# Kernel optimization log

Hardware: AMD Instinct MI355X
Metric: run time of the kernel (lower is better)

## Reference

```python
import jax
import jax.numpy as jnp
import numpy as np
from jax import lax

B, L, A, C = 32, 128, 64, 128  # batch, length, n_agents, channels (in == out)
KT = 3                          # temporal kernel size, padding (KT-1)//2 keeps length


def setup_inputs() -> dict:
    key = jax.random.key(0)
    k1, k2, k3 = jax.random.split(key, 3)
    x = jax.random.normal(k1, (B, L, A, C), dtype=jnp.float32)
    # Conv2d weight [out_ch, in_ch, kt, 1] and bias, kaiming-ish scale
    W = jax.random.normal(k2, (C, C, KT, 1), dtype=jnp.float32) * (1.0 / np.sqrt(C * KT))
    b = jax.random.normal(k3, (C,), dtype=jnp.float32) * 0.01
    return {"x": x, "W": W, "b": b}


def reference(x, W, b):
    # x: [B, L, A, C] -> [B, C, L, A] (torch NCHW layout with H=time, W=agents)
    length, n_agents = x.shape[1], x.shape[2]
    xc = jnp.transpose(x, (0, 3, 1, 2))
    res = xc  # residual is identity (input_dim == output_dim, t_stride == 1)
    pad_t = (KT - 1) // 2
    y = lax.conv_general_dilated(
        xc, W,
        window_strides=(1, 1),
        padding=[(pad_t, pad_t), (0, 0)],
        dimension_numbers=("NCHW", "OIHW", "NCHW"),
    ) + b[None, :, None, None]  # [B, C, L, A]
    # Dense graph g[t,a,t',a'] = 1 iff t==t' or a==a'.  einsum('ncv,vw->ncw', x, g)
    # is exactly: sum over same time (all agents) + sum over same agent (all times) - self.
    agent_sum = jnp.sum(y, axis=3, keepdims=True)  # [B, C, L, 1]
    time_sum = jnp.sum(y, axis=2, keepdims=True)   # [B, C, 1, A]
    scale = (length + n_agents - 2) ** 0.5
    g = (agent_sum + time_sum - y) / scale
    out = jax.nn.relu(g + res)
    return jnp.transpose(out, (0, 2, 3, 1))  # [B, L, A, C]
```

## Files before the change

### kernel.cpp

```cpp
#include <hip/hip_runtime.h>
#include <stdint.h>


typedef __attribute__((ext_vector_type(8))) short bf16x8;
typedef __attribute__((ext_vector_type(4))) float f32x4;

__device__ __forceinline__ uint32_t f2bf(float f) {
    union { float f; uint32_t u; } v; v.f = f;
    return (v.u + 0x7FFFu + ((v.u >> 16) & 1u)) >> 16;
}
__device__ __forceinline__ float bf2f(uint32_t h) {
    union { uint32_t u; float f; } v; v.u = h << 16; return v.f;
}
__device__ __forceinline__ uint32_t pk2(float lo, float hi) {
    return f2bf(lo) | (f2bf(hi) << 16);
}
__device__ __forceinline__ void gll16(const void* g, void* l) {
    __builtin_amdgcn_global_load_lds((const __attribute__((address_space(1))) void*)g,
                                     (__attribute__((address_space(3))) void*)l, 16, 0, 0);
}

__global__ __launch_bounds__(256) void prep_kernel(
    const float* __restrict__ x, uint16_t* __restrict__ x16, uint16_t* __restrict__ xa16,
    const float* __restrict__ W, uint16_t* __restrict__ wp, float* __restrict__ xt)
{
    const int tid = threadIdx.x;
    const int bid = blockIdx.x;
    if (bid >= 4352) {
        const int idx = bid - 4352;
        const int a = idx & 63, b = idx >> 6;
        const int ci8 = (tid & 15) * 8, tg = tid >> 4;
        const float* base = x + ((size_t)(b * 128 + tg) * 64 + a) * 128 + ci8;
        float s[8];
        #pragma unroll
        for (int j = 0; j < 8; ++j) s[j] = 0.f;
        #pragma unroll
        for (int r = 0; r < 8; ++r) {
            const float* p = base + (size_t)r * 16 * 8192;
            const float4 v0 = *(const float4*)p;
            const float4 v1 = *(const float4*)(p + 4);
            s[0] += v0.x; s[1] += v0.y; s[2] += v0.z; s[3] += v0.w;
            s[4] += v1.x; s[5] += v1.y; s[6] += v1.z; s[7] += v1.w;
        }
        __shared__ float redx[16][128];
        *(float4*)&redx[tg][ci8]     = make_float4(s[0], s[1], s[2], s[3]);
        *(float4*)&redx[tg][ci8 + 4] = make_float4(s[4], s[5], s[6], s[7]);
        __syncthreads();
        if (tid < 128) {
            float v = 0.f;
            #pragma unroll
            for (int i = 0; i < 16; ++i) v += redx[i][tid];
            xt[(size_t)idx * 128 + tid] = v;
        }
        return;
    }
    if (bid >= 4160) {
        int o = (bid - 4160) * 256 + tid;
        int i = o & 7, lane = (o >> 3) & 63, nt = (o >> 9) & 7, ks = (o >> 12) & 3, d = o >> 14;
        int ci = ks * 32 + (lane >> 4) * 8 + i;
        int co = nt * 16 + (lane & 15);
        wp[o] = (uint16_t)f2bf(W[(co * 128 + ci) * 3 + d]);
        return;
    }
    const int b = bid / 130, tp = bid - b * 130;
    uint16_t* xo = x16 + (size_t)bid * 8192;
    if (tp == 0 || tp == 129) {
        const uint4 z = make_uint4(0, 0, 0, 0);
        #pragma unroll
        for (int k = 0; k < 4; ++k) *(uint4*)(xo + tid * 32 + k * 8) = z;
        if (tid < 16) *(uint4*)(xa16 + (size_t)bid * 128 + tid * 8) = z;
        return;
    }
    const int t = tp - 1;
    const int ci8 = (tid & 15) * 8, ag = tid >> 4;
    const float* xr = x + (size_t)(b * 128 + t) * 8192;
    float s[8];
    #pragma unroll
    for (int j = 0; j < 8; ++j) s[j] = 0.f;
    #pragma unroll
    for (int r = 0; r < 4; ++r) {
        const int a = ag * 4 + r;
        const float4 v0 = *(const float4*)(xr + a * 128 + ci8);
        const float4 v1 = *(const float4*)(xr + a * 128 + ci8 + 4);
        s[0] += v0.x; s[1] += v0.y; s[2] += v0.z; s[3] += v0.w;
        s[4] += v1.x; s[5] += v1.y; s[6] += v1.z; s[7] += v1.w;
        uint4 p;
        p.x = pk2(v0.x, v0.y); p.y = pk2(v0.z, v0.w);
        p.z = pk2(v1.x, v1.y); p.w = pk2(v1.z, v1.w);
        *(uint4*)(xo + a * 128 + ci8) = p;
    }
    __shared__ float red[16][128];
    *(float4*)&red[ag][ci8]     = make_float4(s[0], s[1], s[2], s[3]);
    *(float4*)&red[ag][ci8 + 4] = make_float4(s[4], s[5], s[6], s[7]);
    __syncthreads();
    if (tid < 128) {
        float v = 0.f;
        #pragma unroll
        for (int i = 0; i < 16; ++i) v += red[i][tid];
        xa16[(size_t)bid * 128 + tid] = (uint16_t)f2bf(v);
    }
}

__global__ __launch_bounds__(256, 2) void sums_kernel(
    const uint16_t* __restrict__ xa16, const float* __restrict__ xt,
    const uint16_t* __restrict__ x16, const uint16_t* __restrict__ wp,
    const float* __restrict__ bias, float* __restrict__ asum, float* __restrict__ tsum)
{
    __shared__ __align__(16) uint16_t slab[130 * 128];
    const int tid = threadIdx.x;
    const int lane = tid & 63, wid = tid >> 6;
    const int wm = wid >> 1, wn = wid & 1;
    const int lr = lane & 15, lg = lane >> 4;
    f32x4 acc[4][4];
    #pragma unroll
    for (int mi = 0; mi < 4; ++mi)
        #pragma unroll
        for (int ni = 0; ni < 4; ++ni) acc[mi][ni] = (f32x4)0.f;

    if (blockIdx.x < 32) {
        const int b = blockIdx.x;
        #pragma unroll
        for (int it = 0; it < 9; ++it) {
            const int gg = it * 256 + tid;
            if (gg < 2080) {
                const int row = gg >> 4, sp = gg & 15;
                const int sl = sp ^ (row & 7);
                *(uint4*)(slab + gg * 8) =
                    *(const uint4*)(xa16 + (size_t)(b * 130 + row) * 128 + sl * 8);
            }
        }
        __syncthreads();
        #pragma unroll
        for (int g = 0; g < 4; ++g)
            #pragma unroll
            for (int d = 0; d < 3; ++d) {
                bf16x8 bq[4], af[4];
                #pragma unroll
                for (int ni = 0; ni < 4; ++ni)
                    bq[ni] = *(const bf16x8*)(wp + (size_t)((((d * 4 + g) * 8) + wn * 4 + ni) * 64 + lane) * 8);
                #pragma unroll
                for (int mi = 0; mi < 4; ++mi) {
                    const int row = wm * 64 + mi * 16 + lr + d;
                    af[mi] = *(const bf16x8*)(slab + row * 128 + ((g * 4 + lg) ^ (row & 7)) * 8);
                }
                #pragma unroll
                for (int mi = 0; mi < 4; ++mi)
                    #pragma unroll
                    for (int ni = 0; ni < 4; ++ni)
                        acc[mi][ni] = __builtin_amdgcn_mfma_f32_16x16x32_bf16(af[mi], bq[ni], acc[mi][ni], 0, 0, 0);
            }
        #pragma unroll
        for (int ni = 0; ni < 4; ++ni) {
            const int col = wn * 64 + ni * 16 + lr;
            const float bv = 64.f * bias[col];
            #pragma unroll
            for (int mi = 0; mi < 4; ++mi)
                #pragma unroll
                for (int j = 0; j < 4; ++j) {
                    const int t = wm * 64 + mi * 16 + lg * 4 + j;
                    asum[((size_t)b * 128 + t) * 128 + col] = acc[mi][ni][j] + bv;
                }
        }
        return;
    }

    const int bid = blockIdx.x - 32;
    const int r = tid >> 1, h = tid & 1;
    const int grow = bid * 128 + r, sb = grow >> 6, sa = grow & 63;
    #pragma unroll
    for (int d = 0; d < 3; ++d) {
        {
            const float* Sp = xt + (size_t)grow * 128 + h * 64;
            const uint16_t* Ep = x16 + ((size_t)(sb * 130 + (d == 0 ? 128 : 1)) * 64 + sa) * 128 + h * 64;
            #pragma unroll
            for (int k = 0; k < 8; ++k) {
                float4 f0 = *(const float4*)(Sp + k * 8);
                float4 f1 = *(const float4*)(Sp + k * 8 + 4);
                if (d != 1) {
                    const uint4 e = *(const uint4*)(Ep + k * 8);
                    f0.x -= bf2f(e.x & 0xFFFFu); f0.y -= bf2f(e.x >> 16);
                    f0.z -= bf2f(e.y & 0xFFFFu); f0.w -= bf2f(e.y >> 16);
                    f1.x -= bf2f(e.z & 0xFFFFu); f1.y -= bf2f(e.z >> 16);
                    f1.z -= bf2f(e.w & 0xFFFFu); f1.w -= bf2f(e.w >> 16);
                }
                uint4 o;
                o.x = pk2(f0.x, f0.y); o.y = pk2(f0.z, f0.w);
                o.z = pk2(f1.x, f1.y); o.w = pk2(f1.z, f1.w);
                const int sl = h * 8 + k;
                *(uint4*)(slab + r * 128 + (sl ^ (r & 7)) * 8) = o;
            }
        }
        __syncthreads();
        #pragma unroll
        for (int g = 0; g < 4; ++g) {
            bf16x8 bq[4], af[4];
            #pragma unroll
            for (int ni = 0; ni < 4; ++ni)
                bq[ni] = *(const bf16x8*)(wp + (size_t)((((d * 4 + g) * 8) + wn * 4 + ni) * 64 + lane) * 8);
            #pragma unroll
            for (int mi = 0; mi < 4; ++mi) {
                const int row = wm * 64 + mi * 16 + lr;
                af[mi] = *(const bf16x8*)(slab + row * 128 + ((g * 4 + lg) ^ (row & 7)) * 8);
            }
            #pragma unroll
            for (int mi = 0; mi < 4; ++mi)
                #pragma unroll
                for (int ni = 0; ni < 4; ++ni)
                    acc[mi][ni] = __builtin_amdgcn_mfma_f32_16x16x32_bf16(af[mi], bq[ni], acc[mi][ni], 0, 0, 0);
        }
        __syncthreads();
    }
    #pragma unroll
    for (int ni = 0; ni < 4; ++ni) {
        const int col = wn * 64 + ni * 16 + lr;
        const float bv = 128.f * bias[col];
        #pragma unroll
        for (int mi = 0; mi < 4; ++mi)
            #pragma unroll
            for (int j = 0; j < 4; ++j) {
                const int rg = bid * 128 + wm * 64 + mi * 16 + lg * 4 + j;
                tsum[(size_t)rg * 128 + col] = acc[mi][ni][j] + bv;
            }
    }
}

__global__ __launch_bounds__(512, 6) void conv_kernel(
    const uint16_t* __restrict__ x16, const uint16_t* __restrict__ wp,
    const float* __restrict__ bias, const float* __restrict__ asum,
    const float* __restrict__ tsum, float* __restrict__ out)
{
    __shared__ __align__(16) uint16_t slab[2][192 * 64];
    const int tid = threadIdx.x;
    const int raw = blockIdx.x;
    const int bid = (raw & 7) * 512 + (raw >> 3);
    const int b = bid >> 7, t = bid & 127;
    const int lane = tid & 63, wid = tid >> 6;
    const int lr = lane & 15, lg = lane >> 4;

    f32x4 acc[4];
    #pragma unroll
    for (int mi = 0; mi < 4; ++mi) acc[mi] = (f32x4)0.f;

#define STAGE(c) do {                                                          \
    _Pragma("unroll")                                                          \
    for (int k = 0; k < 3; ++k) {                                              \
        const int row = wid * 24 + k * 8 + (lane >> 3);                        \
        const int gran = (lane & 7) ^ (row & 7);                               \
        const uint16_t* src = x16 +                                            \
            ((size_t)((b * 130 + t + (row >> 6)) * 64 + (row & 63))) * 128 +   \
            (c) * 64 + gran * 8;                                               \
        gll16(src, &slab[c][wid * 1536 + k * 512]);                            \
    } } while (0)

#define MFMA_CHUNK(c) do {                                                     \
    _Pragma("unroll")                                                          \
    for (int d = 0; d < 3; ++d)                                                \
        _Pragma("unroll")                                                      \
        for (int g2 = 0; g2 < 2; ++g2) {                                       \
            const int ks = (c) * 2 + g2;                                       \
            bf16x8 bq, af[4];                                                  \
            bq = *(const bf16x8*)(wp +                                         \
                (size_t)((((d * 4 + ks) * 8) + wid) * 64 + lane) * 8);         \
            _Pragma("unroll")                                                  \
            for (int mi = 0; mi < 4; ++mi) {                                   \
                const int row = d * 64 + mi * 16 + lr;                         \
                af[mi] = *(const bf16x8*)(&slab[c][row * 64 +                  \
                    (((g2 * 4 + lg) ^ (row & 7)) * 8)]);                       \
            }                                                                  \
            _Pragma("unroll")                                                  \
            for (int mi = 0; mi < 4; ++mi)                                     \
                acc[mi] = __builtin_amdgcn_mfma_f32_16x16x32_bf16(             \
                    af[mi], bq, acc[mi], 0, 0, 0);                             \
        } } while (0)

    STAGE(0);
    __syncthreads();
    STAGE(1);
    MFMA_CHUNK(0);
    __syncthreads();
    MFMA_CHUNK(1);
    __syncthreads();

#undef STAGE
#undef MFMA_CHUNK

    {
        const int col = wid * 16 + lr;
        const float bv = bias[col];
        const int cbuf = col >> 6, cl = col & 63;
        #pragma unroll
        for (int mi = 0; mi < 4; ++mi)
            #pragma unroll
            for (int j = 0; j < 4; ++j) {
                const int a = mi * 16 + lg * 4 + j;
                slab[cbuf][a * 64 + (cl ^ ((a & 7) << 3))] = (uint16_t)f2bf(acc[mi][j] + bv);
            }
    }
    __syncthreads();

    {
        const float inv = 0.07254762501100116f;
        const int cg = tid & 15, rb = tid >> 4;
        const int cbuf = cg >> 3, cl8 = (cg & 7) * 8;
        const float* ap = asum + ((size_t)(b * 128 + t)) * 128 + cg * 8;
        const float4 as0 = *(const float4*)ap, as1 = *(const float4*)(ap + 4);
        const float av[8] = {as0.x, as0.y, as0.z, as0.w, as1.x, as1.y, as1.z, as1.w};
        #pragma unroll
        for (int j = 0; j < 2; ++j) {
            const int a = j * 32 + rb;
            const int swz = cl8 ^ ((a & 7) << 3);
            const uint4 yv = *(const uint4*)(&slab[cbuf][a * 64 + swz]);
            const uint4 xv = *(const uint4*)(&slab[cbuf][(64 + a) * 64 + swz]);
            const float* tp = tsum + ((size_t)(b * 64 + a)) * 128 + cg * 8;
            const float4 ts0 = *(const float4*)tp, ts1 = *(const float4*)(tp + 4);
            float yy[8], xx[8];
            yy[0] = bf2f(yv.x & 0xFFFFu); yy[1] = bf2f(yv.x >> 16);
            yy[2] = bf2f(yv.y & 0xFFFFu); yy[3] = bf2f(yv.y >> 16);
            yy[4] = bf2f(yv.z & 0xFFFFu); yy[5] = bf2f(yv.z >> 16);
            yy[6] = bf2f(yv.w & 0xFFFFu); yy[7] = bf2f(yv.w >> 16);
            xx[0] = bf2f(xv.x & 0xFFFFu); xx[1] = bf2f(xv.x >> 16);
            xx[2] = bf2f(xv.y & 0xFFFFu); xx[3] = bf2f(xv.y >> 16);
            xx[4] = bf2f(xv.z & 0xFFFFu); xx[5] = bf2f(xv.z >> 16);
            xx[6] = bf2f(xv.w & 0xFFFFu); xx[7] = bf2f(xv.w >> 16);
            const float tv[8] = {ts0.x, ts0.y, ts0.z, ts0.w, ts1.x, ts1.y, ts1.z, ts1.w};
            float o[8];
            #pragma unroll
            for (int i = 0; i < 8; ++i) {
                const float gg = (av[i] + tv[i] - yy[i]) * inv + xx[i];
                o[i] = gg > 0.f ? gg : 0.f;
            }
            float* op = out + ((size_t)((b * 128 + t) * 64 + a)) * 128 + cg * 8;
            *(float4*)op       = make_float4(o[0], o[1], o[2], o[3]);
            *(float4*)(op + 4) = make_float4(o[4], o[5], o[6], o[7]);
        }
    }
}

extern "C" void kernel_launch(void* const* d_in, const int* in_sizes, int n_in,
                              void* d_out, int out_size, void* d_ws, size_t ws_size,
                              hipStream_t stream) {
    const float* x    = (const float*)d_in[0];
    const float* W    = (const float*)d_in[1];
    const float* bias = (const float*)d_in[2];
    float* out = (float*)d_out;

    char* ws = (char*)d_ws;
    uint16_t* x16  = (uint16_t*)(ws);
    uint16_t* wp   = (uint16_t*)(ws + 68157440);
    uint16_t* xa16 = (uint16_t*)(ws + 68157440 + 98304);
    float* xt      = (float*)(ws + 68157440 + 98304 + 1064960);
    float* asum    = (float*)(ws + 68157440 + 98304 + 1064960 + 1048576);
    float* tsum    = (float*)(ws + 68157440 + 98304 + 1064960 + 1048576 + 2097152);

    prep_kernel <<<6400, 256, 0, stream>>>(x, x16, xa16, W, wp, xt);
    sums_kernel <<<48,   256, 0, stream>>>(xa16, xt, x16, wp, bias, asum, tsum);
    conv_kernel <<<4096, 512, 0, stream>>>(x16, wp, bias, asum, tsum, out);
}
```

Measured before the change: 129.7 us.

## Drop bf16 copy of input; convert fp32 to bf16 inside conv staging

Removes the intermediate bf16 padded copy of x, so the conv kernel loads fp32 x directly and converts it to bf16 while staging into LDS, with zeros for the time-padding rows. The time and agent reductions are fused into a single pass over x that writes per-group partial time sums, followed by a small second-stage reduction kernel. This is meant to eliminate the large write and re-read of x16 and a duplicate read of x. In exchange, conv reads twice as many bytes per tile and gives up the async global-to-LDS loads in favour of register loads plus LDS stores.

```diff
diff --git a/kernel.cpp b/kernel.cpp
--- a/kernel.cpp
+++ b/kernel.cpp
@@ -15,95 +15,96 @@
 __device__ __forceinline__ uint32_t pk2(float lo, float hi) {
     return f2bf(lo) | (f2bf(hi) << 16);
 }
-__device__ __forceinline__ void gll16(const void* g, void* l) {
-    __builtin_amdgcn_global_load_lds((const __attribute__((address_space(1))) void*)g,
-                                     (__attribute__((address_space(3))) void*)l, 16, 0, 0);
-}
-
-__global__ __launch_bounds__(256) void prep_kernel(
-    const float* __restrict__ x, uint16_t* __restrict__ x16, uint16_t* __restrict__ xa16,
-    const float* __restrict__ W, uint16_t* __restrict__ wp, float* __restrict__ xt)
+
+__global__ __launch_bounds__(256) void red_kernel(
+    const float* __restrict__ x, uint16_t* __restrict__ xa16, float* __restrict__ xt_part,
+    const float* __restrict__ W, uint16_t* __restrict__ wp)
 {
     const int tid = threadIdx.x;
     const int bid = blockIdx.x;
-    if (bid >= 4352) {
-        const int idx = bid - 4352;
-        const int a = idx & 63, b = idx >> 6;
-        const int ci8 = (tid & 15) * 8, tg = tid >> 4;
-        const float* base = x + ((size_t)(b * 128 + tg) * 64 + a) * 128 + ci8;
-        float s[8];
-        #pragma unroll
-        for (int j = 0; j < 8; ++j) s[j] = 0.f;
-        #pragma unroll
-        for (int r = 0; r < 8; ++r) {
-            const float* p = base + (size_t)r * 16 * 8192;
-            const float4 v0 = *(const float4*)p;
-            const float4 v1 = *(const float4*)(p + 4);
-            s[0] += v0.x; s[1] += v0.y; s[2] += v0.z; s[3] += v0.w;
-            s[4] += v1.x; s[5] += v1.y; s[6] += v1.z; s[7] += v1.w;
-        }
-        __shared__ float redx[16][128];
-        *(float4*)&redx[tg][ci8]     = make_float4(s[0], s[1], s[2], s[3]);
-        *(float4*)&redx[tg][ci8 + 4] = make_float4(s[4], s[5], s[6], s[7]);
-        __syncthreads();
-        if (tid < 128) {
-            float v = 0.f;
-            #pragma unroll
-            for (int i = 0; i < 16; ++i) v += redx[i][tid];
-            xt[(size_t)idx * 128 + tid] = v;
-        }
-        return;
-    }
-    if (bid >= 4160) {
-        int o = (bid - 4160) * 256 + tid;
+    if (bid >= 512) {
+        int o = (bid - 512) * 256 + tid;
         int i = o & 7, lane = (o >> 3) & 63, nt = (o >> 9) & 7, ks = (o >> 12) & 3, d = o >> 14;
         int ci = ks * 32 + (lane >> 4) * 8 + i;
         int co = nt * 16 + (lane & 15);
         wp[o] = (uint16_t)f2bf(W[(co * 128 + ci) * 3 + d]);
         return;
     }
-    const int b = bid / 130, tp = bid - b * 130;
-    uint16_t* xo = x16 + (size_t)bid * 8192;
-    if (tp == 0 || tp == 129) {
-        const uint4 z = make_uint4(0, 0, 0, 0);
-        #pragma unroll
-        for (int k = 0; k < 4; ++k) *(uint4*)(xo + tid * 32 + k * 8) = z;
-        if (tid < 16) *(uint4*)(xa16 + (size_t)bid * 128 + tid * 8) = z;
-        return;
-    }
-    const int t = tp - 1;
+    const int b = bid >> 4, g = bid & 15;
     const int ci8 = (tid & 15) * 8, ag = tid >> 4;
-    const float* xr = x + (size_t)(b * 128 + t) * 8192;
+    __shared__ float red[16][128];
+
+    float xtl[4][8];
+    #pragma unroll
+    for (int r = 0; r < 4; ++r)
+        #pragma unroll
+        for (int j = 0; j < 8; ++j) xtl[r][j] = 0.f;
+
+    #pragma unroll
+    for (int ti = 0; ti < 8; ++ti) {
+        const int t = g * 8 + ti;
+        const float* xr = x + ((size_t)(b * 128 + t) * 64) * 128;
+        float s[8];
+        #pragma unroll
+        for (int j = 0; j < 8; ++j) s[j] = 0.f;
+        #pragma unroll
+        for (int r = 0; r < 4; ++r) {
+            const int a = ag * 4 + r;
+            const float4 v0 = *(const float4*)(xr + a * 128 + ci8);
+            const float4 v1 = *(const float4*)(xr + a * 128 + ci8 + 4);
+            s[0] += v0.x; s[1] += v0.y; s[2] += v0.z; s[3] += v0.w;
+            s[4] += v1.x; s[5] += v1.y; s[6] += v1.z; s[7] += v1.w;
+            xtl[r][0] += v0.x; xtl[r][1] += v0.y; xtl[r][2] += v0.z; xtl[r][3] += v0.w;
+            xtl[r][4] += v1.x; xtl[r][5] += v1.y; xtl[r][6] += v1.z; xtl[r][7] += v1.w;
+        }
+        *(float4*)&red[ag][ci8]     = make_float4(s[0], s[1], s[2], s[3]);
+        *(float4*)&red[ag][ci8 + 4] = make_float4(s[4], s[5], s[6], s[7]);
+        __syncthreads();
+        if (tid < 128) {
+            float v = 0.f;
+            #pragma unroll
+            for (int i = 0; i < 16; ++i) v += red[i][tid];
+            xa16[(size_t)(b * 130 + t + 1) * 128 + tid] = (uint16_t)f2bf(v);
+        }
+        __syncthreads();
+    }
+    if (g == 0 && tid < 16)
+        *(uint4*)(xa16 + (size_t)(b * 130) * 128 + tid * 8) = make_uint4(0, 0, 0, 0);
+    if (g == 15 && tid < 16)
+        *(uint4*)(xa16 + (size_t)(b * 130 + 129) * 128 + tid * 8) = make_uint4(0, 0, 0, 0);
+    #pragma unroll
+    for (int r = 0; r < 4; ++r) {
+        float* p = xt_part + (((size_t)(b * 16 + g) * 64 + ag * 4 + r) * 128) + ci8;
+        *(float4*)p       = make_float4(xtl[r][0], xtl[r][1], xtl[r][2], xtl[r][3]);
+        *(float4*)(p + 4) = make_float4(xtl[r][4], xtl[r][5], xtl[r][6], xtl[r][7]);
+    }
+}
+
+__global__ __launch_bounds__(256) void xtr_kernel(
+    const float* __restrict__ xt_part, float* __restrict__ xt)
+{
+    const int idx = blockIdx.x * 256 + threadIdx.x;
+    const int row = idx >> 4, ci8 = (idx & 15) * 8;
+    const int b = row >> 6, a = row & 63;
     float s[8];
     #pragma unroll
     for (int j = 0; j < 8; ++j) s[j] = 0.f;
     #pragma unroll
-    for (int r = 0; r < 4; ++r) {
-        const int a = ag * 4 + r;
-        const float4 v0 = *(const float4*)(xr + a * 128 + ci8);
-        const float4 v1 = *(const float4*)(xr + a * 128 + ci8 + 4);
+    for (int g2 = 0; g2 < 16; ++g2) {
+        const float* p = xt_part + (((size_t)(b * 16 + g2) * 64 + a) * 128) + ci8;
+        const float4 v0 = *(const float4*)p;
+        const float4 v1 = *(const float4*)(p + 4);
         s[0] += v0.x; s[1] += v0.y; s[2] += v0.z; s[3] += v0.w;
         s[4] += v1.x; s[5] += v1.y; s[6] += v1.z; s[7] += v1.w;
-        uint4 p;
-        p.x = pk2(v0.x, v0.y); p.y = pk2(v0.z, v0.w);
-        p.z = pk2(v1.x, v1.y); p.w = pk2(v1.z, v1.w);
-        *(uint4*)(xo + a * 128 + ci8) = p;
-    }
-    __shared__ float red[16][128];
-    *(float4*)&red[ag][ci8]     = make_float4(s[0], s[1], s[2], s[3]);
-    *(float4*)&red[ag][ci8 + 4] = make_float4(s[4], s[5], s[6], s[7]);
-    __syncthreads();
-    if (tid < 128) {
-        float v = 0.f;
-        #pragma unroll
-        for (int i = 0; i < 16; ++i) v += red[i][tid];
-        xa16[(size_t)bid * 128 + tid] = (uint16_t)f2bf(v);
-    }
+    }
+    float* q = xt + (size_t)row * 128 + ci8;
+    *(float4*)q       = make_float4(s[0], s[1], s[2], s[3]);
+    *(float4*)(q + 4) = make_float4(s[4], s[5], s[6], s[7]);
 }
 
 __global__ __launch_bounds__(256, 2) void sums_kernel(
     const uint16_t* __restrict__ xa16, const float* __restrict__ xt,
-    const uint16_t* __restrict__ x16, const uint16_t* __restrict__ wp,
+    const float* __restrict__ x, const uint16_t* __restrict__ wp,
     const float* __restrict__ bias, float* __restrict__ asum, float* __restrict__ tsum)
 {
     __shared__ __align__(16) uint16_t slab[130 * 128];
@@ -171,17 +172,16 @@
     for (int d = 0; d < 3; ++d) {
         {
             const float* Sp = xt + (size_t)grow * 128 + h * 64;
-            const uint16_t* Ep = x16 + ((size_t)(sb * 130 + (d == 0 ? 128 : 1)) * 64 + sa) * 128 + h * 64;
+            const float* Ep = x + ((size_t)((sb * 128 + (d == 0 ? 127 : 0)) * 64 + sa)) * 128 + h * 64;
             #pragma unroll
             for (int k = 0; k < 8; ++k) {
                 float4 f0 = *(const float4*)(Sp + k * 8);
                 float4 f1 = *(const float4*)(Sp + k * 8 + 4);
                 if (d != 1) {
-                    const uint4 e = *(const uint4*)(Ep + k * 8);
-                    f0.x -= bf2f(e.x & 0xFFFFu); f0.y -= bf2f(e.x >> 16);
-                    f0.z -= bf2f(e.y & 0xFFFFu); f0.w -= bf2f(e.y >> 16);
-                    f1.x -= bf2f(e.z & 0xFFFFu); f1.y -= bf2f(e.z >> 16);
-                    f1.z -= bf2f(e.w & 0xFFFFu); f1.w -= bf2f(e.w >> 16);
+                    const float4 e0 = *(const float4*)(Ep + k * 8);
+                    const float4 e1 = *(const float4*)(Ep + k * 8 + 4);
+                    f0.x -= e0.x; f0.y -= e0.y; f0.z -= e0.z; f0.w -= e0.w;
+                    f1.x -= e1.x; f1.y -= e1.y; f1.z -= e1.z; f1.w -= e1.w;
                 }
                 uint4 o;
                 o.x = pk2(f0.x, f0.y); o.y = pk2(f0.z, f0.w);
@@ -225,7 +225,7 @@
 }
 
 __global__ __launch_bounds__(512, 6) void conv_kernel(
-    const uint16_t* __restrict__ x16, const uint16_t* __restrict__ wp,
+    const float* __restrict__ x, const uint16_t* __restrict__ wp,
     const float* __restrict__ bias, const float* __restrict__ asum,
     const float* __restrict__ tsum, float* __restrict__ out)
 {
@@ -244,12 +244,21 @@
 #define STAGE(c) do {                                                          \
     _Pragma("unroll")                                                          \
     for (int k = 0; k < 3; ++k) {                                              \
-        const int row = wid * 24 + k * 8 + (lane >> 3);                        \
-        const int gran = (lane & 7) ^ (row & 7);                               \
-        const uint16_t* src = x16 +                                            \
-            ((size_t)((b * 130 + t + (row >> 6)) * 64 + (row & 63))) * 128 +   \
-            (c) * 64 + gran * 8;                                               \
-        gll16(src, &slab[c][wid * 1536 + k * 512]);                            \
+        const int ro  = lane >> 3;                                             \
+        const int row = wid * 24 + k * 8 + ro;                                 \
+        const int gl  = (lane & 7) ^ ro;                                       \
+        const int tloc = t + (row >> 6) - 1;                                   \
+        uint4 o4 = make_uint4(0, 0, 0, 0);                                     \
+        if ((unsigned)tloc < 128u) {                                           \
+            const float* s_ = x +                                              \
+                ((size_t)((b * 128 + tloc) * 64 + (row & 63))) * 128 +         \
+                (c) * 64 + gl * 8;                                             \
+            const float4 v0 = *(const float4*)s_;                              \
+            const float4 v1 = *(const float4*)(s_ + 4);                        \
+            o4.x = pk2(v0.x, v0.y); o4.y = pk2(v0.z, v0.w);                    \
+            o4.z = pk2(v1.x, v1.y); o4.w = pk2(v1.z, v1.w);                    \
+        }                                                                      \
+        *(uint4*)(&slab[c][wid * 1536 + k * 512 + lane * 8]) = o4;             \
     } } while (0)
 
 #define MFMA_CHUNK(c) do {                                                     \
@@ -345,14 +354,15 @@
     float* out = (float*)d_out;
 
     char* ws = (char*)d_ws;
-    uint16_t* x16  = (uint16_t*)(ws);
-    uint16_t* wp   = (uint16_t*)(ws + 68157440);
-    uint16_t* xa16 = (uint16_t*)(ws + 68157440 + 98304);
-    float* xt      = (float*)(ws + 68157440 + 98304 + 1064960);
-    float* asum    = (float*)(ws + 68157440 + 98304 + 1064960 + 1048576);
-    float* tsum    = (float*)(ws + 68157440 + 98304 + 1064960 + 1048576 + 2097152);
-
-    prep_kernel <<<6400, 256, 0, stream>>>(x, x16, xa16, W, wp, xt);
-    sums_kernel <<<48,   256, 0, stream>>>(xa16, xt, x16, wp, bias, asum, tsum);
-    conv_kernel <<<4096, 512, 0, stream>>>(x16, wp, bias, asum, tsum, out);
-}
+    uint16_t* wp    = (uint16_t*)(ws);
+    uint16_t* xa16  = (uint16_t*)(ws + 98304);
+    float* xt_part  = (float*)(ws + 98304 + 1064960);
+    float* xt       = (float*)(ws + 98304 + 1064960 + 16777216);
+    float* asum     = (float*)(ws + 98304 + 1064960 + 16777216 + 1048576);
+    float* tsum     = (float*)(ws + 98304 + 1064960 + 16777216 + 1048576 + 2097152);
+
+    red_kernel  <<<704,  256, 0, stream>>>(x, xa16, xt_part, W, wp);
+    xtr_kernel  <<<128,  256, 0, stream>>>(xt_part, xt);
+    sums_kernel <<<48,   256, 0, stream>>>(xa16, xt, x, wp, bias, asum, tsum);
+    conv_kernel <<<4096, 512, 0, stream>>>(x, wp, bias, asum, tsum, out);
+}
```

Result: faster. 114.9 us (-11.5%).
